# Performance work log

Hardware: AMD Instinct MI355X
Metric: run time of the kernel (lower is better)

The kernel has to match this reference:

```python
import jax, jax.numpy as jnp
import numpy as np

I_DIM = 512   # encoder feature size fed to CfC
UNITS = 1024  # AutoNCP total units (hidden_dim)
OUT = 128     # motor neurons (output_dim)
N = [538, 358, 128]                      # inter, command, motor layer sizes
IN_TOT = [I_DIM + N[0], N[0] + N[1], N[1] + N[2]]  # concat(input, h) width per layer
B, T = 512, 128


def setup_inputs() -> dict:
    key = jax.random.key(0)
    ks = jax.random.split(key, 40)
    d = {}
    d["x"] = jax.random.normal(ks[0], (B, T, I_DIM), jnp.float32)
    d["h0"] = jnp.zeros((B, UNITS), jnp.float32)
    ki = 1
    for l in range(3):
        it, n = IN_TOT[l], N[l]
        sp = (jax.random.uniform(ks[ki], (n, it - n)) < 0.5).astype(jnp.float32); ki += 1
        d[f"mask{l}"] = jnp.concatenate([sp, jnp.ones((n, n), jnp.float32)], axis=1)
        for name in ("Wff1", "Wff2", "Wta", "Wtb"):
            d[f"{name}_{l}"] = jax.random.normal(ks[ki], (n, it), jnp.float32) * float(1.0 / np.sqrt(it)); ki += 1
        for name in ("bff1", "bff2", "bta", "btb"):
            d[f"{name}_{l}"] = jnp.zeros((n,), jnp.float32)
    d["Wfc"] = jax.random.normal(ks[ki], (OUT, OUT), jnp.float32) * float(1.0 / np.sqrt(OUT))
    d["bfc"] = jnp.zeros((OUT,), jnp.float32)
    return d


def _cell(xin, h, p):
    # CfCCell, mode='default', no backbone, ts = 1.0
    W1, b1, W2, b2, Wa, ba, Wb, bb = p
    xc = jnp.concatenate([xin, h], axis=-1)           # (B, in+n)
    ff1 = jnp.tanh(xc @ W1.T + b1)
    ff2 = jnp.tanh(xc @ W2.T + b2)
    t_interp = jax.nn.sigmoid((xc @ Wa.T + ba) + (xc @ Wb.T + bb))
    return ff1 * (1.0 - t_interp) + t_interp * ff2


def reference(x, h0, mask0, Wff1_0, Wff2_0, Wta_0, Wtb_0, bff1_0, bff2_0, bta_0, btb_0,
              mask1, Wff1_1, Wff2_1, Wta_1, Wtb_1, bff1_1, bff2_1, bta_1, btb_1,
              mask2, Wff1_2, Wff2_2, Wta_2, Wtb_2, bff1_2, bff2_2, bta_2, btb_2,
              Wfc, bfc):
    params = (
        (Wff1_0 * mask0, bff1_0, Wff2_0 * mask0, bff2_0, Wta_0, bta_0, Wtb_0, btb_0),
        (Wff1_1 * mask1, bff1_1, Wff2_1 * mask1, bff2_1, Wta_1, bta_1, Wtb_1, btb_1),
        (Wff1_2 * mask2, bff1_2, Wff2_2 * mask2, bff2_2, Wta_2, bta_2, Wtb_2, btb_2),
    )
    hs0 = tuple(jnp.split(h0, [N[0], N[0] + N[1]], axis=1))

    def step(hs, x_t):
        inp = x_t
        new = []
        for l in range(3):
            inp = _cell(inp, hs[l], params[l])
            new.append(inp)
        return tuple(new), inp  # last layer (motor) is the cell output

    carry, outs = jax.lax.scan(step, hs0, jnp.swapaxes(x, 0, 1))
    outputs = jnp.swapaxes(outs, 0, 1)        # (B, T, OUT)
    hn = jnp.concatenate(carry, axis=1)       # (B, UNITS)
    predictions = outputs @ Wfc.T + bfc       # final nn.Linear
    return predictions, hn
```

## Files before the change

### kernel.cpp

```cpp
#include <hip/hip_runtime.h>
#include <stdint.h>

typedef __attribute__((ext_vector_type(8))) short short8;
typedef __attribute__((ext_vector_type(4))) float float4v;
typedef __attribute__((ext_vector_type(4))) unsigned short ushort4v;

constexpr int T = 128;
constexpr int NB = 512;
constexpr int NCH = 16;
constexpr int CBLK = 12;

__device__ __forceinline__ float bf2f(ushort u) {
  union { float f; uint32_t i; } v; v.i = ((uint32_t)u) << 16; return v.f;
}
__device__ __forceinline__ ushort f2bf(float f) {
  union { float f; uint32_t i; } v; v.f = f;
  uint32_t i = v.i;
  uint32_t r = i + 0x7FFFu + ((i >> 16) & 1u);
  return (ushort)(r >> 16);
}

__device__ __forceinline__ float coh_load(const float* p) {
  return __hip_atomic_load(const_cast<float*>(p), __ATOMIC_RELAXED,
                           __HIP_MEMORY_SCOPE_SYSTEM);
}
__device__ __forceinline__ void coh_store(float* p, float v) {
  __hip_atomic_store(p, v, __ATOMIC_RELAXED, __HIP_MEMORY_SCOPE_SYSTEM);
}

__global__ __launch_bounds__(256) void pack_w(const float* __restrict__ W,
                                              const float* __restrict__ mask,
                                              ushort* __restrict__ out, int loOff,
                                              int NN, int IT, int NT, int KB) {
  int idx = blockIdx.x * 256 + threadIdx.x;
  int total = KB * NT * 512;
  if (idx >= total) return;
  int jj   = idx & 7;
  int lane = (idx >> 3) & 63;
  int nt   = (idx >> 9) % NT;
  int kb   = (idx >> 9) / NT;
  int n = nt * 16 + (lane & 15);
  int k = kb * 32 + (lane >> 4) * 8 + jj;
  float v = 0.f;
  if (n < NN && k < IT) {
    v = W[(size_t)n * IT + k];
    if (mask) v *= mask[(size_t)n * IT + k];
  }
  ushort hi = f2bf(v);
  out[idx] = hi;
  out[loOff + idx] = f2bf(v - bf2f(hi));
}

template <int NTW, bool C0, bool C1, int KB>
__device__ __forceinline__ void cell_job(
    ushort* __restrict__ Ah, ushort* __restrict__ Al, float* __restrict__ Acc,
    const float* __restrict__ a0, int a0s, const float* __restrict__ a1, int a1s,
    int SEG1, int IT, int NT, int loOff,
    const ushort* const* __restrict__ wf4, const float* const* __restrict__ bias4,
    int NN, float* __restrict__ hout, float* __restrict__ out2,
    int b0, int ntp) {
  constexpr int PD = 4;
  const int tid  = threadIdx.x;
  const int wave = tid >> 6, lane = tid & 63, quad = lane >> 4, l16 = lane & 15;
  const ushort* wfq = wf4[wave];
  const int nt0 = ntp * NTW;
  const int n0  = nt0 * 16;

  float4v acc[2][NTW];
#pragma unroll
  for (int i = 0; i < 2; i++)
#pragma unroll
    for (int w = 0; w < NTW; w++) acc[i][w] = float4v{0.f, 0.f, 0.f, 0.f};

  const int sm = tid >> 3;
  const int sk = (tid & 7) * 4;
  const size_t ar0 = (size_t)(b0 + sm) * a0s;
  const size_t ar1 = (size_t)(b0 + sm) * a1s;

  short8 cbh[PD][NTW], cbl[PD][NTW];
  float4v av[PD];

  auto loadB = [&](int kb, short8* bh, short8* bl) {
#pragma unroll
    for (int w = 0; w < NTW; w++) {
      const size_t fo = ((size_t)(kb * NT + nt0 + w) * 64 + lane) * 8;
      bh[w] = *(const short8*)(wfq + fo);
      bl[w] = *(const short8*)(wfq + loOff + fo);
    }
  };
  auto loadA = [&](int kb) -> float4v {
    const int kg0 = kb * 32 + sk;
    float4v r;
    if (!C0 && kg0 + 3 < SEG1) {
      r = *(const float4v*)(a0 + ar0 + kg0);
    } else {
#pragma unroll
      for (int e = 0; e < 4; e++) {
        int kg = kg0 + e;
        float v = 0.f;
        if (kg < SEG1)    v = C0 ? coh_load(a0 + ar0 + kg) : a0[ar0 + kg];
        else if (kg < IT) v = C1 ? coh_load(a1 + ar1 + (kg - SEG1)) : a1[ar1 + (kg - SEG1)];
        r[e] = v;
      }
    }
    return r;
  };

#pragma unroll
  for (int i = 0; i < PD; i++) { av[i] = loadA(i); loadB(i, cbh[i], cbl[i]); }

  for (int kb0 = 0; kb0 < KB; kb0 += PD) {
#pragma unroll
    for (int u = 0; u < PD; u++) {
      const int kb = kb0 + u;
      if ((KB % PD) && kb >= KB) continue;
      const int ab = (u & 1) * 1280;

      ushort4v hi4, lo4;
#pragma unroll
      for (int e = 0; e < 4; e++) {
        float v = av[u][e];
        ushort hi = f2bf(v);
        hi4[e] = hi;
        lo4[e] = f2bf(v - bf2f(hi));
      }
      *(ushort4v*)(Ah + ab + sm * 40 + sk) = hi4;
      *(ushort4v*)(Al + ab + sm * 40 + sk) = lo4;
      asm volatile("s_waitcnt lgkmcnt(0)\n\ts_barrier" ::: "memory");

#pragma unroll
      for (int mt = 0; mt < 2; mt++) {
        short8 ah = *(const short8*)&Ah[ab + (mt * 16 + l16) * 40 + quad * 8];
        short8 al = *(const short8*)&Al[ab + (mt * 16 + l16) * 40 + quad * 8];
#pragma unroll
        for (int w = 0; w < NTW; w++) {
          acc[mt][w] = __builtin_amdgcn_mfma_f32_16x16x32_bf16(ah, cbh[u][w], acc[mt][w], 0, 0, 0);
          acc[mt][w] = __builtin_amdgcn_mfma_f32_16x16x32_bf16(al, cbh[u][w], acc[mt][w], 0, 0, 0);
          acc[mt][w] = __builtin_amdgcn_mfma_f32_16x16x32_bf16(ah, cbl[u][w], acc[mt][w], 0, 0, 0);
        }
      }
      if (kb + PD < KB) { av[u] = loadA(kb + PD); loadB(kb + PD, cbh[u], cbl[u]); }
    }
  }

#pragma unroll
  for (int mt = 0; mt < 2; mt++)
#pragma unroll
    for (int w = 0; w < NTW; w++)
#pragma unroll
      for (int r = 0; r < 4; r++) {
        int row = mt * 16 + quad * 4 + r;
        int col = w * 16 + l16;
        Acc[(wave * 32 + row) * 50 + col] = acc[mt][w][r];
      }
  __syncthreads();

  const int CW = 16 * NTW;
  for (int idx = tid; idx < 32 * CW; idx += 256) {
    int r = idx / CW, c = idx % CW;
    int j = n0 + c;
    if (j >= NN) continue;
    float v1 = Acc[(0 * 32 + r) * 50 + c] + bias4[0][j];
    float v2 = Acc[(1 * 32 + r) * 50 + c] + bias4[1][j];
    float va = Acc[(2 * 32 + r) * 50 + c] + bias4[2][j];
    float vb = Acc[(3 * 32 + r) * 50 + c] + bias4[3][j];
    float ff1 = tanhf(v1);
    float ff2 = tanhf(v2);
    float s = 1.f / (1.f + expf(-(va + vb)));
    float h = ff1 * (1.f - s) + s * ff2;
    size_t b = (size_t)(b0 + r);
    coh_store(hout + b * 1024 + j, h);
    if (out2) out2[b * 16384 + j] = h;
  }
}

struct PParams {
  const float* x;
  float* h0; float* h1;
  const ushort* wf0[4]; const ushort* wf1[4]; const ushort* wf2[4];
  int loOff0, loOff1, loOff2;
  const float* bias0[4]; const float* bias1[4]; const float* bias2[4];
  float* pred;
  int* bar;
};

__device__ __forceinline__ void chain_barrier(int* slot, int target) {
  asm volatile("s_waitcnt vmcnt(0)" ::: "memory");
  __syncthreads();
  if (threadIdx.x == 0) {
    __hip_atomic_fetch_add(slot, 1, __ATOMIC_RELAXED, __HIP_MEMORY_SCOPE_SYSTEM);
    while (__hip_atomic_load(slot, __ATOMIC_RELAXED, __HIP_MEMORY_SCOPE_SYSTEM) < target)
      __builtin_amdgcn_s_sleep(1);
  }
  __syncthreads();
}

__global__ __launch_bounds__(256, 1) void cfc_persistent(PParams p) {
  __shared__ ushort Ah[2 * 32 * 40];
  __shared__ ushort Al[2 * 32 * 40];
  __shared__ float  Acc[4 * 32 * 50];
  const int blk = blockIdx.x;
  const int c = blk / CBLK, ntp = blk % CBLK;
  const int b0 = c * 32;
  int* cbar = p.bar + c * (T * 3);

  for (int t = 0; t < T; t++) {
    float* hr = (t & 1) ? p.h1 : p.h0;
    float* hw = (t & 1) ? p.h0 : p.h1;
    cell_job<3, false, true, 33>(Ah, Al, Acc, p.x + (size_t)t * 512, T * 512, hr, 1024,
                                 512, 1050, 36, p.loOff0, p.wf0, p.bias0, 538,
                                 hw, nullptr, b0, ntp);
    chain_barrier(cbar + t * 3, CBLK);
    cell_job<2, true, true, 28>(Ah, Al, Acc, hw, 1024, hr + 538, 1024,
                                538, 896, 24, p.loOff1, p.wf1, p.bias1, 358,
                                hw + 538, nullptr, b0, ntp);
    chain_barrier(cbar + t * 3 + 1, CBLK);
    if (ntp < 4) {
      cell_job<2, true, true, 16>(Ah, Al, Acc, hw + 538, 1024, hr + 896, 1024,
                                  358, 486, 8, p.loOff2, p.wf2, p.bias2, 128,
                                  hw + 896, p.pred + (size_t)t * 128, b0, ntp);
      chain_barrier(cbar + t * 3 + 2, 4);
    }
  }
}

__global__ __launch_bounds__(256)
void final_linear(float* __restrict__ io, const ushort* __restrict__ wfc_frag,
                  int loOff, const float* __restrict__ bfc) {
  __shared__ ushort Ah[64][136];
  __shared__ ushort Al[64][136];
  const int tid = threadIdx.x;
  const int wave = tid >> 6, lane = tid & 63, quad = lane >> 4, l16 = lane & 15;
  const size_t r0 = (size_t)blockIdx.x * 64;
  {
    const int row = tid >> 2;
    const int cb  = (tid & 3) * 32;
    const float* src = io + (r0 + row) * 128 + cb;
#pragma unroll
    for (int e = 0; e < 32; e++) {
      float v = src[e];
      ushort hi = f2bf(v);
      Ah[row][cb + e] = hi;
      Al[row][cb + e] = f2bf(v - bf2f(hi));
    }
  }
  __syncthreads();
  float4v acc[8];
#pragma unroll
  for (int i = 0; i < 8; i++) acc[i] = float4v{0.f, 0.f, 0.f, 0.f};
#pragma unroll
  for (int kb = 0; kb < 4; kb++) {
    short8 ah = *(const short8*)&Ah[wave * 16 + l16][kb * 32 + quad * 8];
    short8 al = *(const short8*)&Al[wave * 16 + l16][kb * 32 + quad * 8];
#pragma unroll
    for (int nt = 0; nt < 8; nt++) {
      const size_t fo = ((size_t)(kb * 8 + nt) * 64 + lane) * 8;
      short8 bh = *(const short8*)(wfc_frag + fo);
      short8 bl = *(const short8*)(wfc_frag + loOff + fo);
      acc[nt] = __builtin_amdgcn_mfma_f32_16x16x32_bf16(ah, bh, acc[nt], 0, 0, 0);
      acc[nt] = __builtin_amdgcn_mfma_f32_16x16x32_bf16(al, bh, acc[nt], 0, 0, 0);
      acc[nt] = __builtin_amdgcn_mfma_f32_16x16x32_bf16(ah, bl, acc[nt], 0, 0, 0);
    }
  }
  __syncthreads();
#pragma unroll
  for (int nt = 0; nt < 8; nt++) {
    int col = nt * 16 + l16;
    float bb = bfc[col];
#pragma unroll
    for (int r = 0; r < 4; r++) {
      int row = wave * 16 + quad * 4 + r;
      io[(r0 + row) * 128 + col] = acc[nt][r] + bb;
    }
  }
}

extern "C" void kernel_launch(void* const* d_in, const int* in_sizes, int n_in,
                              void* d_out, int out_size, void* d_ws, size_t ws_size,
                              hipStream_t stream) {
  const int maskIdx[3] = {2, 11, 20};
  const int wIdx[3]    = {3, 12, 21};
  const float* Wfc = (const float*)d_in[29];
  const float* bfc = (const float*)d_in[30];

  const int KBs[3] = {33, 28, 16};
  const int NTs[3] = {36, 24, 8};
  const int NNs[3] = {538, 358, 128};
  const int ITs[3] = {1050, 896, 486};

  ushort* ws = (ushort*)d_ws;
  size_t off = 0;
  ushort* wf[3][4];
  int loOff[3];
  for (int l = 0; l < 3; l++) {
    loOff[l] = KBs[l] * NTs[l] * 512;
    for (int q = 0; q < 4; q++) {
      wf[l][q] = ws + off;
      off += (size_t)2 * loOff[l];
    }
  }
  int wfcLo = 4 * 8 * 512;
  ushort* wfc_f = ws + off; off += (size_t)2 * wfcLo;
  float* hb0 = (float*)(ws + off); off += (size_t)NB * 1024 * 2;
  float* hb1 = (float*)(ws + off); off += (size_t)NB * 1024 * 2;
  int* bar = (int*)(ws + off); off += (size_t)NCH * T * 3 * 2;

  float* pred = (float*)d_out;
  float* hn   = (float*)d_out + (size_t)NB * T * 128;

  for (int l = 0; l < 3; l++) {
    int blocks = (loOff[l] + 255) / 256;
    for (int q = 0; q < 4; q++) {
      const float* m = (q < 2) ? (const float*)d_in[maskIdx[l]] : nullptr;
      pack_w<<<blocks, 256, 0, stream>>>((const float*)d_in[wIdx[l] + q], m, wf[l][q],
                                         loOff[l], NNs[l], ITs[l], NTs[l], KBs[l]);
    }
  }
  pack_w<<<(wfcLo + 255) / 256, 256, 0, stream>>>(Wfc, nullptr, wfc_f, wfcLo, 128, 128, 8, 4);

  hipMemsetAsync(bar, 0, NCH * T * 3 * sizeof(int), stream);
  hipMemcpyAsync(hb0, d_in[1], (size_t)NB * 1024 * sizeof(float),
                 hipMemcpyDeviceToDevice, stream);

  PParams p;
  p.x = (const float*)d_in[0];
  p.h0 = hb0; p.h1 = hb1;
  for (int q = 0; q < 4; q++) {
    p.wf0[q] = wf[0][q]; p.wf1[q] = wf[1][q]; p.wf2[q] = wf[2][q];
    p.bias0[q] = (const float*)d_in[7 + q];
    p.bias1[q] = (const float*)d_in[16 + q];
    p.bias2[q] = (const float*)d_in[25 + q];
  }
  p.loOff0 = loOff[0]; p.loOff1 = loOff[1]; p.loOff2 = loOff[2];
  p.pred = pred;
  p.bar = bar;

  cfc_persistent<<<NCH * CBLK, 256, 0, stream>>>(p);

  final_linear<<<(NB * T) / 64, 256, 0, stream>>>(pred, wfc_f, wfcLo, bfc);
  hipMemcpyAsync(hn, hb0, (size_t)NB * 1024 * sizeof(float),
                 hipMemcpyDeviceToDevice, stream);
}
```

Before: 6.635 ms.

## Pad hidden-state layout and overlap recurrent K-range with barrier waits

```diff
diff --git a/kernel.cpp b/kernel.cpp
--- a/kernel.cpp
+++ b/kernel.cpp
@@ -9,6 +9,7 @@
 constexpr int NB = 512;
 constexpr int NCH = 16;
 constexpr int CBLK = 12;
+constexpr int HS = 1056;
 
 __device__ __forceinline__ float bf2f(ushort u) {
   union { float f; uint32_t i; } v; v.i = ((uint32_t)u) << 16; return v.f;
@@ -20,18 +21,23 @@
   return (ushort)(r >> 16);
 }
 
-__device__ __forceinline__ float coh_load(const float* p) {
-  return __hip_atomic_load(const_cast<float*>(p), __ATOMIC_RELAXED,
-                           __HIP_MEMORY_SCOPE_SYSTEM);
-}
-__device__ __forceinline__ void coh_store(float* p, float v) {
-  __hip_atomic_store(p, v, __ATOMIC_RELAXED, __HIP_MEMORY_SCOPE_SYSTEM);
+__device__ __forceinline__ unsigned long long coh_load8(const float* p) {
+  return __hip_atomic_load(
+      reinterpret_cast<unsigned long long*>(const_cast<float*>(p)),
+      __ATOMIC_RELAXED, __HIP_MEMORY_SCOPE_SYSTEM);
+}
+__device__ __forceinline__ void coh_store8(float* p, float a, float b) {
+  union { unsigned long long u; float f[2]; } v; v.f[0] = a; v.f[1] = b;
+  __hip_atomic_store(reinterpret_cast<unsigned long long*>(p), v.u,
+                     __ATOMIC_RELAXED, __HIP_MEMORY_SCOPE_SYSTEM);
 }
 
 __global__ __launch_bounds__(256) void pack_w(const float* __restrict__ W,
                                               const float* __restrict__ mask,
                                               ushort* __restrict__ out, int loOff,
-                                              int NN, int IT, int NT, int KB) {
+                                              int NN, int IT, int NT, int KB,
+                                              int POLD, int OLDLEN, int SOFF,
+                                              int NEWLEN) {
   int idx = blockIdx.x * 256 + threadIdx.x;
   int total = KB * NT * 512;
   if (idx >= total) return;
@@ -40,42 +46,36 @@
   int nt   = (idx >> 9) % NT;
   int kb   = (idx >> 9) / NT;
   int n = nt * 16 + (lane & 15);
-  int k = kb * 32 + (lane >> 4) * 8 + jj;
+  int p = kb * 32 + (lane >> 4) * 8 + jj;
+  int src = -1;
+  if (p < POLD) {
+    if (p < OLDLEN) src = SOFF + p;
+  } else {
+    int q = p - POLD;
+    if (q < NEWLEN) src = q;
+  }
   float v = 0.f;
-  if (n < NN && k < IT) {
-    v = W[(size_t)n * IT + k];
-    if (mask) v *= mask[(size_t)n * IT + k];
+  if (n < NN && src >= 0) {
+    v = W[(size_t)n * IT + src];
+    if (mask) v *= mask[(size_t)n * IT + src];
   }
   ushort hi = f2bf(v);
   out[idx] = hi;
   out[loOff + idx] = f2bf(v - bf2f(hi));
 }
 
-template <int NTW, bool C0, bool C1, int KB>
-__device__ __forceinline__ void cell_job(
-    ushort* __restrict__ Ah, ushort* __restrict__ Al, float* __restrict__ Acc,
-    const float* __restrict__ a0, int a0s, const float* __restrict__ a1, int a1s,
-    int SEG1, int IT, int NT, int loOff,
-    const ushort* const* __restrict__ wf4, const float* const* __restrict__ bias4,
-    int NN, float* __restrict__ hout, float* __restrict__ out2,
-    int b0, int ntp) {
+template <int NTW, bool COH, int KB0, int KB1, int KOFF>
+__device__ __forceinline__ void cell_range(
+    ushort* __restrict__ Ah, ushort* __restrict__ Al,
+    const float* __restrict__ aRow,
+    const ushort* __restrict__ wfq, int nt0, int NT, int loOff,
+    float4v (&acc)[2][NTW]) {
   constexpr int PD = 4;
+  constexpr int LEN = KB1 - KB0;
   const int tid  = threadIdx.x;
-  const int wave = tid >> 6, lane = tid & 63, quad = lane >> 4, l16 = lane & 15;
-  const ushort* wfq = wf4[wave];
-  const int nt0 = ntp * NTW;
-  const int n0  = nt0 * 16;
-
-  float4v acc[2][NTW];
-#pragma unroll
-  for (int i = 0; i < 2; i++)
-#pragma unroll
-    for (int w = 0; w < NTW; w++) acc[i][w] = float4v{0.f, 0.f, 0.f, 0.f};
-
+  const int lane = tid & 63, quad = lane >> 4, l16 = lane & 15;
   const int sm = tid >> 3;
   const int sk = (tid & 7) * 4;
-  const size_t ar0 = (size_t)(b0 + sm) * a0s;
-  const size_t ar1 = (size_t)(b0 + sm) * a1s;
 
   short8 cbh[PD][NTW], cbl[PD][NTW];
   float4v av[PD];
@@ -89,32 +89,28 @@
     }
   };
   auto loadA = [&](int kb) -> float4v {
-    const int kg0 = kb * 32 + sk;
+    const float* p = aRow + (kb - KOFF) * 32 + sk;
     float4v r;
-    if (!C0 && kg0 + 3 < SEG1) {
-      r = *(const float4v*)(a0 + ar0 + kg0);
+    if (COH) {
+      union { unsigned long long u; float f[2]; } x0, x1;
+      x0.u = coh_load8(p);
+      x1.u = coh_load8(p + 2);
+      r[0] = x0.f[0]; r[1] = x0.f[1]; r[2] = x1.f[0]; r[3] = x1.f[1];
     } else {
-#pragma unroll
-      for (int e = 0; e < 4; e++) {
-        int kg = kg0 + e;
-        float v = 0.f;
-        if (kg < SEG1)    v = C0 ? coh_load(a0 + ar0 + kg) : a0[ar0 + kg];
-        else if (kg < IT) v = C1 ? coh_load(a1 + ar1 + (kg - SEG1)) : a1[ar1 + (kg - SEG1)];
-        r[e] = v;
-      }
+      r = *(const float4v*)p;
     }
     return r;
   };
 
 #pragma unroll
-  for (int i = 0; i < PD; i++) { av[i] = loadA(i); loadB(i, cbh[i], cbl[i]); }
-
-  for (int kb0 = 0; kb0 < KB; kb0 += PD) {
+  for (int i = 0; i < PD; i++) { av[i] = loadA(KB0 + i); loadB(KB0 + i, cbh[i], cbl[i]); }
+
+  for (int kb0 = KB0; kb0 < KB1; kb0 += PD) {
 #pragma unroll
     for (int u = 0; u < PD; u++) {
       const int kb = kb0 + u;
-      if ((KB % PD) && kb >= KB) continue;
-      const int ab = (u & 1) * 1280;
+      if ((LEN % PD) && kb >= KB1) continue;
+      const int ab = (kb & 1) * 1280;
 
       ushort4v hi4, lo4;
 #pragma unroll
@@ -139,38 +135,57 @@
           acc[mt][w] = __builtin_amdgcn_mfma_f32_16x16x32_bf16(ah, cbl[u][w], acc[mt][w], 0, 0, 0);
         }
       }
-      if (kb + PD < KB) { av[u] = loadA(kb + PD); loadB(kb + PD, cbh[u], cbl[u]); }
-    }
-  }
-
+      if (kb + PD < KB1) { av[u] = loadA(kb + PD); loadB(kb + PD, cbh[u], cbl[u]); }
+    }
+  }
+}
+
+template <int NTW>
+__device__ __forceinline__ void cell_epilogue(
+    float* __restrict__ Acc, float4v (&acc)[2][NTW],
+    const float* const* __restrict__ bias4,
+    int NN, int NNPAD, float* __restrict__ hout, float* __restrict__ out2,
+    int b0, int n0) {
+  const int tid = threadIdx.x;
+  const int wave = tid >> 6, lane = tid & 63, quad = lane >> 4, l16 = lane & 15;
 #pragma unroll
   for (int mt = 0; mt < 2; mt++)
 #pragma unroll
     for (int w = 0; w < NTW; w++)
 #pragma unroll
-      for (int r = 0; r < 4; r++) {
-        int row = mt * 16 + quad * 4 + r;
-        int col = w * 16 + l16;
-        Acc[(wave * 32 + row) * 50 + col] = acc[mt][w][r];
+      for (int r = 0; r < 4; r++)
+        Acc[(wave * 32 + mt * 16 + quad * 4 + r) * 50 + w * 16 + l16] = acc[mt][w][r];
+  __syncthreads();
+  constexpr int CW = 16 * NTW;
+  for (int i4 = tid; i4 < 32 * (CW / 4); i4 += 256) {
+    const int r = i4 / (CW / 4);
+    const int c4 = (i4 % (CW / 4)) * 4;
+    const int j0 = n0 + c4;
+    if (j0 >= NNPAD) continue;
+    float hv[4];
+#pragma unroll
+    for (int e = 0; e < 4; e++) {
+      const int c = c4 + e, j = j0 + e;
+      float h = 0.f;
+      if (j < NN) {
+        float v1 = Acc[(0 * 32 + r) * 50 + c] + bias4[0][j];
+        float v2 = Acc[(1 * 32 + r) * 50 + c] + bias4[1][j];
+        float va = Acc[(2 * 32 + r) * 50 + c] + bias4[2][j];
+        float vb = Acc[(3 * 32 + r) * 50 + c] + bias4[3][j];
+        float ff1 = tanhf(v1);
+        float ff2 = tanhf(v2);
+        float s = 1.f / (1.f + expf(-(va + vb)));
+        h = ff1 * (1.f - s) + s * ff2;
       }
-  __syncthreads();
-
-  const int CW = 16 * NTW;
-  for (int idx = tid; idx < 32 * CW; idx += 256) {
-    int r = idx / CW, c = idx % CW;
-    int j = n0 + c;
-    if (j >= NN) continue;
-    float v1 = Acc[(0 * 32 + r) * 50 + c] + bias4[0][j];
-    float v2 = Acc[(1 * 32 + r) * 50 + c] + bias4[1][j];
-    float va = Acc[(2 * 32 + r) * 50 + c] + bias4[2][j];
-    float vb = Acc[(3 * 32 + r) * 50 + c] + bias4[3][j];
-    float ff1 = tanhf(v1);
-    float ff2 = tanhf(v2);
-    float s = 1.f / (1.f + expf(-(va + vb)));
-    float h = ff1 * (1.f - s) + s * ff2;
-    size_t b = (size_t)(b0 + r);
-    coh_store(hout + b * 1024 + j, h);
-    if (out2) out2[b * 16384 + j] = h;
+      hv[e] = h;
+    }
+    float* hp = hout + (size_t)(b0 + r) * HS + j0;
+    coh_store8(hp, hv[0], hv[1]);
+    coh_store8(hp + 2, hv[2], hv[3]);
+    if (out2) {
+      float4v o; o[0] = hv[0]; o[1] = hv[1]; o[2] = hv[2]; o[3] = hv[3];
+      *(float4v*)(out2 + (size_t)(b0 + r) * 16384 + j0) = o;
+    }
   }
 }
 
@@ -184,11 +199,14 @@
   int* bar;
 };
 
-__device__ __forceinline__ void chain_barrier(int* slot, int target) {
+__device__ __forceinline__ void bar_arrive(int* slot) {
   asm volatile("s_waitcnt vmcnt(0)" ::: "memory");
   __syncthreads();
+  if (threadIdx.x == 0)
+    __hip_atomic_fetch_add(slot, 1, __ATOMIC_RELAXED, __HIP_MEMORY_SCOPE_SYSTEM);
+}
+__device__ __forceinline__ void bar_wait(int* slot, int target) {
   if (threadIdx.x == 0) {
-    __hip_atomic_fetch_add(slot, 1, __ATOMIC_RELAXED, __HIP_MEMORY_SCOPE_SYSTEM);
     while (__hip_atomic_load(slot, __ATOMIC_RELAXED, __HIP_MEMORY_SCOPE_SYSTEM) < target)
       __builtin_amdgcn_s_sleep(1);
   }
@@ -203,25 +221,74 @@
   const int c = blk / CBLK, ntp = blk % CBLK;
   const int b0 = c * 32;
   int* cbar = p.bar + c * (T * 3);
+  const int wave = threadIdx.x >> 6;
+  const int sm = threadIdx.x >> 3;
+  const size_t rowoff = (size_t)(b0 + sm);
 
   for (int t = 0; t < T; t++) {
     float* hr = (t & 1) ? p.h1 : p.h0;
     float* hw = (t & 1) ? p.h0 : p.h1;
-    cell_job<3, false, true, 33>(Ah, Al, Acc, p.x + (size_t)t * 512, T * 512, hr, 1024,
-                                 512, 1050, 36, p.loOff0, p.wf0, p.bias0, 538,
-                                 hw, nullptr, b0, ntp);
-    chain_barrier(cbar + t * 3, CBLK);
-    cell_job<2, true, true, 28>(Ah, Al, Acc, hw, 1024, hr + 538, 1024,
-                                538, 896, 24, p.loOff1, p.wf1, p.bias1, 358,
-                                hw + 538, nullptr, b0, ntp);
-    chain_barrier(cbar + t * 3 + 1, CBLK);
+    const float* xRow  = p.x + rowoff * (T * 512) + (size_t)t * 512;
+    const float* hrRow = hr + rowoff * HS;
+    const float* hwRow = hw + rowoff * HS;
+
+    float4v acc0[2][3];
+#pragma unroll
+    for (int i = 0; i < 2; i++)
+#pragma unroll
+      for (int w = 0; w < 3; w++) acc0[i][w] = float4v{0.f, 0.f, 0.f, 0.f};
+    cell_range<3, false, 0, 16, 0 >(Ah, Al, xRow,  p.wf0[wave], ntp * 3, 36, p.loOff0, acc0);
+    cell_range<3, true, 16, 33, 16>(Ah, Al, hrRow, p.wf0[wave], ntp * 3, 36, p.loOff0, acc0);
+    cell_epilogue<3>(Acc, acc0, p.bias0, 538, 544, hw, nullptr, b0, ntp * 48);
+    bar_arrive(cbar + t * 3);
+
+    if (t && ntp >= 4) bar_wait(cbar + (t - 1) * 3 + 1, CBLK);
+    float4v acc1[2][2];
+#pragma unroll
+    for (int i = 0; i < 2; i++)
+#pragma unroll
+      for (int w = 0; w < 2; w++) acc1[i][w] = float4v{0.f, 0.f, 0.f, 0.f};
+    cell_range<2, true, 0, 12, 0 >(Ah, Al, hrRow + 544, p.wf1[wave], ntp * 2, 24, p.loOff1, acc1);
+    bar_wait(cbar + t * 3, CBLK);
+    cell_range<2, true, 12, 29, 12>(Ah, Al, hwRow, p.wf1[wave], ntp * 2, 24, p.loOff1, acc1);
+    cell_epilogue<2>(Acc, acc1, p.bias1, 358, 384, hw + 544, nullptr, b0, ntp * 32);
+    bar_arrive(cbar + t * 3 + 1);
+
     if (ntp < 4) {
-      cell_job<2, true, true, 16>(Ah, Al, Acc, hw + 538, 1024, hr + 896, 1024,
-                                  358, 486, 8, p.loOff2, p.wf2, p.bias2, 128,
-                                  hw + 896, p.pred + (size_t)t * 128, b0, ntp);
-      chain_barrier(cbar + t * 3 + 2, 4);
-    }
-  }
+      if (t) bar_wait(cbar + (t - 1) * 3 + 2, 4);
+      float4v acc2[2][2];
+#pragma unroll
+      for (int i = 0; i < 2; i++)
+#pragma unroll
+        for (int w = 0; w < 2; w++) acc2[i][w] = float4v{0.f, 0.f, 0.f, 0.f};
+      cell_range<2, true, 0, 4, 0>(Ah, Al, hrRow + 928, p.wf2[wave], ntp * 2, 8, p.loOff2, acc2);
+      bar_wait(cbar + t * 3 + 1, CBLK);
+      cell_range<2, true, 4, 16, 4>(Ah, Al, hwRow + 544, p.wf2[wave], ntp * 2, 8, p.loOff2, acc2);
+      cell_epilogue<2>(Acc, acc2, p.bias2, 128, 128, hw + 928,
+                       p.pred + (size_t)t * 128, b0, ntp * 32);
+      bar_arrive(cbar + t * 3 + 2);
+    }
+  }
+}
+
+__global__ __launch_bounds__(256) void h_scatter(const float* __restrict__ src,
+                                                 float* __restrict__ dst) {
+  int idx = blockIdx.x * 256 + threadIdx.x;
+  if (idx >= NB * HS) return;
+  int b = idx / HS, u = idx % HS;
+  int s = -1;
+  if (u < 538) s = u;
+  else if (u >= 544 && u < 902) s = 538 + (u - 544);
+  else if (u >= 928) s = 896 + (u - 928);
+  dst[idx] = (s >= 0) ? src[(size_t)b * 1024 + s] : 0.f;
+}
+__global__ __launch_bounds__(256) void h_gather(const float* __restrict__ src,
+                                                float* __restrict__ dst) {
+  int idx = blockIdx.x * 256 + threadIdx.x;
+  if (idx >= NB * 1024) return;
+  int b = idx / 1024, u = idx % 1024;
+  int pu = (u < 538) ? u : (u < 896 ? (u - 538) + 544 : (u - 896) + 928);
+  dst[idx] = src[(size_t)b * HS + pu];
 }
 
 __global__ __launch_bounds__(256)
@@ -283,10 +350,14 @@
   const float* Wfc = (const float*)d_in[29];
   const float* bfc = (const float*)d_in[30];
 
-  const int KBs[3] = {33, 28, 16};
-  const int NTs[3] = {36, 24, 8};
-  const int NNs[3] = {538, 358, 128};
-  const int ITs[3] = {1050, 896, 486};
+  const int KBs[3]  = {33, 29, 16};
+  const int NTs[3]  = {36, 24, 8};
+  const int NNs[3]  = {538, 358, 128};
+  const int ITs[3]  = {1050, 896, 486};
+  const int POLDs[3]   = {0, 384, 128};
+  const int OLDLENs[3] = {0, 358, 128};
+  const int SOFFs[3]   = {0, 538, 358};
+  const int NEWLENs[3] = {1050, 538, 358};
 
   ushort* ws = (ushort*)d_ws;
   size_t off = 0;
@@ -301,8 +372,8 @@
   }
   int wfcLo = 4 * 8 * 512;
   ushort* wfc_f = ws + off; off += (size_t)2 * wfcLo;
-  float* hb0 = (float*)(ws + off); off += (size_t)NB * 1024 * 2;
-  float* hb1 = (float*)(ws + off); off += (size_t)NB * 1024 * 2;
+  float* hb0 = (float*)(ws + off); off += (size_t)NB * HS * 2;
+  float* hb1 = (float*)(ws + off); off += (size_t)NB * HS * 2;
   int* bar = (int*)(ws + off); off += (size_t)NCH * T * 3 * 2;
 
   float* pred = (float*)d_out;
@@ -313,14 +384,15 @@
     for (int q = 0; q < 4; q++) {
       const float* m = (q < 2) ? (const float*)d_in[maskIdx[l]] : nullptr;
       pack_w<<<blocks, 256, 0, stream>>>((const float*)d_in[wIdx[l] + q], m, wf[l][q],
-                                         loOff[l], NNs[l], ITs[l], NTs[l], KBs[l]);
-    }
-  }
-  pack_w<<<(wfcLo + 255) / 256, 256, 0, stream>>>(Wfc, nullptr, wfc_f, wfcLo, 128, 128, 8, 4);
+                                         loOff[l], NNs[l], ITs[l], NTs[l], KBs[l],
+                                         POLDs[l], OLDLENs[l], SOFFs[l], NEWLENs[l]);
+    }
+  }
+  pack_w<<<(wfcLo + 255) / 256, 256, 0, stream>>>(Wfc, nullptr, wfc_f, wfcLo,
+                                                  128, 128, 8, 4, 0, 0, 0, 128);
 
   hipMemsetAsync(bar, 0, NCH * T * 3 * sizeof(int), stream);
-  hipMemcpyAsync(hb0, d_in[1], (size_t)NB * 1024 * sizeof(float),
-                 hipMemcpyDeviceToDevice, stream);
+  h_scatter<<<(NB * HS + 255) / 256, 256, 0, stream>>>((const float*)d_in[1], hb0);
 
   PParams p;
   p.x = (const float*)d_in[0];
@@ -338,6 +410,5 @@
   cfc_persistent<<<NCH * CBLK, 256, 0, stream>>>(p);
 
   final_linear<<<(NB * T) / 64, 256, 0, stream>>>(pred, wfc_f, wfcLo, bfc);
-  hipMemcpyAsync(hn, hb0, (size_t)NB * 1024 * sizeof(float),
-                 hipMemcpyDeviceToDevice, stream);
-}
+  h_gather<<<(NB * 1024 + 255) / 256, 256, 0, stream>>>(hb0, hn);
+}
```

Measured after the change: 5.867 ms. 11.6% less time.
